# Kernel tuning notes

Measured on AMD Instinct MI355X. Metric: run time of the kernel, lower is better.

The kernel has to match this reference:

```python
import jax, jax.numpy as jnp
import numpy as np

MARGIN = 0.075
CONF_THRESHOLD = 0.2


def setup_inputs() -> dict:
    key = jax.random.key(0)
    k1, k2, k3 = jax.random.split(key, 3)
    N, D = 32768, 256
    embeddings = jax.random.normal(k1, (N, D), dtype=jnp.float32)
    tags = jax.random.randint(k2, (N,), 0, 500, dtype=jnp.int64)
    confidences = jax.random.uniform(k3, (N,), dtype=jnp.float32)
    return {"embeddings": embeddings, "tags": tags, "confidences": confidences}


def _safe_sqrt(sq):
    # gradient-safe sqrt: zero at sq<=0 (matches d(0)=0, avoids NaN in vjp)
    pos = sq > 0
    return jnp.where(pos, jnp.sqrt(jnp.where(pos, sq, 1.0)), 0.0)


def _triplet_hard_mining(emb, labels):
    n = emb.shape[0]
    # pairwise euclidean distances (cdist p=2)
    sq_norm = jnp.sum(emb * emb, axis=1)  # [n]
    sq = sq_norm[:, None] + sq_norm[None, :] - 2.0 * (emb @ emb.T)
    dist = _safe_sqrt(jnp.maximum(sq, 0.0))  # [n, n]

    same = labels[:, None] == labels[None, :]
    eye = jnp.eye(n, dtype=bool)
    pos_mask = same & ~eye
    neg_mask = ~same

    inf = jnp.float32(jnp.inf)
    hard_pos = jnp.max(jnp.where(pos_mask, dist, -inf), axis=1)  # [n]
    neg_min = jnp.min(jnp.where(neg_mask, dist, inf), axis=1)    # [n]
    # semi-hard negatives: neg dists strictly greater than hardest positive
    shn_mask = neg_mask & (dist > hard_pos[:, None])
    shn_min = jnp.min(jnp.where(shn_mask, dist, inf), axis=1)
    hard_neg = jnp.where(jnp.isfinite(shn_min), shn_min, neg_min)

    valid = jnp.any(pos_mask, axis=1) & jnp.any(neg_mask, axis=1)
    per_anchor = jax.nn.relu(hard_pos - hard_neg + MARGIN)
    per_anchor = jnp.where(valid, per_anchor, 0.0)
    cnt = jnp.sum(valid.astype(jnp.float32))
    # if no valid anchors (also covers <2 unique labels), loss is 0
    return jnp.where(cnt > 0, jnp.sum(per_anchor) / jnp.maximum(cnt, 1.0), 0.0)


def reference(embeddings, tags, confidences):
    n = embeddings.shape[0]
    top_k = int(CONF_THRESHOLD * n)
    _, idx = jax.lax.top_k(confidences, top_k)
    emb = embeddings[idx]
    labels = tags[idx]
    return _triplet_hard_mining(emb, labels)
```

## Files before the change

kernel.cpp:

```cpp
#include <hip/hip_runtime.h>
#include <math.h>

#define D 256
#define MARGIN 0.075f

typedef __bf16 bf8_t __attribute__((ext_vector_type(8)));
typedef float f4_t __attribute__((ext_vector_type(4)));
typedef unsigned long long ull;

#define AS1 __attribute__((address_space(1)))
#define AS3 __attribute__((address_space(3)))
static __device__ __forceinline__ void gload_lds16(const void* g, void* s) {
    __builtin_amdgcn_global_load_lds((const AS1 unsigned int*)g, (AS3 unsigned int*)s, 16, 0, 0);
}

static __device__ __forceinline__ unsigned short f2bf(float x) {
    unsigned u = __float_as_uint(x);
    unsigned r = (u + 0x7fffu + ((u >> 16) & 1u)) >> 16;
    return (unsigned short)r;
}

static __device__ __forceinline__ float dec_min(unsigned cm) {
    return (cm == 0u) ? __builtin_inff() : __uint_as_float(~cm);
}

__global__ void k_hist1(const float* __restrict__ conf, int n,
                        unsigned* __restrict__ hist) {
    int i = blockIdx.x * blockDim.x + threadIdx.x;
    if (i < n) atomicAdd(&hist[__float_as_uint(conf[i]) >> 16], 1u);
}

__global__ __launch_bounds__(1024) void k_scan(const unsigned* __restrict__ hist,
                                               unsigned* __restrict__ ctrl, int ksel) {
    __shared__ unsigned part[1024];
    __shared__ int schunk;
    int t = threadIdx.x;
    unsigned k = (unsigned)ksel;
    unsigned s = 0;
    const uint4* h4 = (const uint4*)(hist + t * 64);
    #pragma unroll
    for (int b = 0; b < 16; b++) {
        uint4 v = h4[b];
        s += v.x + v.y + v.z + v.w;
    }
    part[t] = s;
    __syncthreads();
    for (int off = 1; off < 1024; off <<= 1) {
        unsigned v = (t + off < 1024) ? part[t + off] : 0u;
        __syncthreads();
        part[t] += v;
        __syncthreads();
    }
    if (part[t] >= k && (t == 1023 || part[t + 1] < k)) schunk = t;
    __syncthreads();
    if (t == 0) {
        int c = schunk;
        unsigned cum = (c == 1023) ? 0u : part[c + 1];
        int bin = 0; unsigned rem = 1;
        for (int b = 63; b >= 0; b--) {
            unsigned h = hist[c * 64 + b];
            if (cum + h >= k) { bin = c * 64 + b; rem = k - cum; break; }
            cum += h;
        }
        ctrl[3] = (unsigned)bin;
        ctrl[1] = k - rem;
        ctrl[2] = rem;
    }
}

__global__ void k_sel(const float* __restrict__ conf, int n,
                      unsigned* __restrict__ ctrl, int* __restrict__ idx_sel,
                      ull* __restrict__ cand) {
    int i = blockIdx.x * blockDim.x + threadIdx.x;
    if (i < n) {
        unsigned u = __float_as_uint(conf[i]);
        unsigned t16 = u >> 16, b16 = ctrl[3];
        if (t16 > b16) {
            unsigned pos = atomicAdd(&ctrl[5], 1u);
            idx_sel[pos] = i;
        } else if (t16 == b16) {
            unsigned pos = atomicAdd(&ctrl[6], 1u);
            cand[pos] = ((ull)u << 32) | (unsigned)i;
        }
    }
}

__global__ __launch_bounds__(256) void k_sel2(const unsigned* __restrict__ ctrl,
                                              const ull* __restrict__ cand,
                                              int* __restrict__ idx_sel) {
    int t = threadIdx.x;
    int M = (int)ctrl[6];
    unsigned need = ctrl[2], cgt = ctrl[1];
    for (int j = t; j < M; j += 256) {
        ull cj = cand[j];
        unsigned rank = 0;
        for (int m = 0; m < M; m++) {
            ull cm = cand[m];
            unsigned um = (unsigned)(cm >> 32), uj = (unsigned)(cj >> 32);
            if (um > uj || (um == uj && cm < cj)) rank++;
        }
        if (rank < need) idx_sel[cgt + rank] = (int)(unsigned)(cj & 0xFFFFFFFFu);
    }
}

__global__ void k_gather(const float* __restrict__ emb, const int* __restrict__ tags,
                         const int* __restrict__ idx_sel, int ksel, int np,
                         unsigned short* __restrict__ ebf, float* __restrict__ sqn,
                         int* __restrict__ lsel, unsigned* __restrict__ labhist) {
    int j = blockIdx.x;
    int t = threadIdx.x;
    if (j < ksel) {
        int src = idx_sel[j];
        float4 v = *(const float4*)&emb[(size_t)src * D + t * 4];
        ushort4 o;
        o.x = f2bf(v.x); o.y = f2bf(v.y); o.z = f2bf(v.z); o.w = f2bf(v.w);
        *(ushort4*)&ebf[(size_t)j * D + t * 4] = o;
        float s = v.x * v.x + v.y * v.y + v.z * v.z + v.w * v.w;
        for (int off = 32; off > 0; off >>= 1) s += __shfl_down(s, off);
        if (t == 0) {
            int lab = tags[src];
            sqn[j] = s; lsel[j] = lab;
            atomicAdd(&labhist[lab], 1u);
        }
    } else {
        ushort4 z = {0, 0, 0, 0};
        *(ushort4*)&ebf[(size_t)j * D + t * 4] = z;
        if (t == 0) { sqn[j] = 0.f; lsel[j] = -1; }
    }
}

template <int PASS>
__global__ __launch_bounds__(256, 3) void k_fused(const unsigned short* __restrict__ Ebf,
                                                  const float* __restrict__ sqn,
                                                  const int* __restrict__ lsel,
                                                  unsigned* __restrict__ hp_g,
                                                  unsigned* __restrict__ nm_g,
                                                  unsigned* __restrict__ shn_g,
                                                  int np, int nb, int ksel) {
    int rem = blockIdx.x, bi = 0;
    while (rem >= nb - bi) { rem -= nb - bi; bi++; }
    int bj = bi + rem;
    int i0 = bi * 128, j0 = bj * 128;
    bool diag = (bi == bj);

    __shared__ __align__(16) char smem[32768];
    char* ldsA = smem;
    char* ldsB = smem + 16384;

    int t = threadIdx.x;
    int w = t >> 6, l = t & 63;
    int wm = w & 1, wn = w >> 1;
    int lr = l & 15, lq = l >> 4;
    int r7 = lr & 7, rh = lr >> 3;

    int dr = l >> 3;
    int sg = (l & 7) ^ dr;
    const unsigned short* gA = Ebf + (size_t)(i0 + dr) * D + sg * 8;
    const unsigned short* gB = Ebf + (size_t)(j0 + dr) * D + sg * 8;

    f4_t zero = {0.f, 0.f, 0.f, 0.f};
    f4_t acc[4][4];
    #pragma unroll
    for (int p = 0; p < 4; p++)
        #pragma unroll
        for (int q = 0; q < 4; q++) acc[p][q] = zero;

    for (int k0 = 0; k0 < D; k0 += 64) {
        #pragma unroll
        for (int c = 0; c < 4; c++) {
            int R0 = w * 32 + c * 8;
            gload_lds16(gA + (size_t)R0 * D + k0, ldsA + R0 * 128);
            gload_lds16(gB + (size_t)R0 * D + k0, ldsB + R0 * 128);
        }
        __syncthreads();
        #pragma unroll
        for (int ks8 = 0; ks8 < 8; ks8 += 4) {
            bf8_t a[4], b[4];
            #pragma unroll
            for (int p = 0; p < 4; p++) {
                int off = ((wm * 8 + p * 2 + rh) << 10) + ((r7 * 8 + (((ks8 + lq)) ^ r7)) << 4);
                a[p] = *(const bf8_t*)(ldsA + off);
            }
            #pragma unroll
            for (int q = 0; q < 4; q++) {
                int off = ((wn * 8 + q * 2 + rh) << 10) + ((r7 * 8 + (((ks8 + lq)) ^ r7)) << 4);
                b[q] = *(const bf8_t*)(ldsB + off);
            }
            #pragma unroll
            for (int p = 0; p < 4; p++)
                #pragma unroll
                for (int q = 0; q < 4; q++)
                    acc[p][q] = __builtin_amdgcn_mfma_f32_16x16x32_bf16(a[p], b[q], acc[p][q], 0, 0, 0);
        }
        __syncthreads();
    }

    float* sqnA = (float*)smem;
    float* sqnB = sqnA + 128;
    int* labA = (int*)(sqnB + 128);
    int* labB = labA + 128;
    float* hpA2 = (float*)(labB + 128);
    float* hpB2 = hpA2 + 128;
    if (t < 128) {
        sqnA[t] = sqn[i0 + t];
        labA[t] = lsel[i0 + t];
        if (PASS == 2) hpA2[t] = __uint_as_float(hp_g[i0 + t]);
    } else {
        int u = t - 128;
        sqnB[u] = sqn[j0 + u];
        labB[u] = lsel[j0 + u];
        if (PASS == 2) hpB2[u] = __uint_as_float(hp_g[j0 + u]);
    }
    __syncthreads();

    const float INF = __builtin_inff();
    float dsq[4][4][4];
    int colL[4], ljv[4];
    #pragma unroll
    for (int q = 0; q < 4; q++) { colL[q] = wn * 64 + q * 16 + lr; ljv[q] = labB[colL[q]]; }
    #pragma unroll
    for (int p = 0; p < 4; p++) {
        #pragma unroll
        for (int r = 0; r < 4; r++) {
            int rowL = wm * 64 + p * 16 + lq * 4 + r;
            int gm = i0 + rowL;
            float smi = sqnA[rowL];
            #pragma unroll
            for (int q = 0; q < 4; q++) {
                int gn = j0 + colL[q];
                float s = fmaxf(smi + sqnB[colL[q]] - 2.f * acc[p][q][r], 0.f);
                dsq[p][q][r] = (gm < ksel && gn < ksel) ? s : INF;
            }
        }
    }

    #pragma unroll
    for (int p = 0; p < 4; p++) {
        #pragma unroll
        for (int r = 0; r < 4; r++) {
            int rowL = wm * 64 + p * 16 + lq * 4 + r;
            int li = labA[rowL];
            if (PASS == 1) {
                float hpv = -INF, nmv = INF;
                #pragma unroll
                for (int q = 0; q < 4; q++) {
                    float d = dsq[p][q][r];
                    bool self = diag && (rowL == colL[q]);
                    if (ljv[q] == li) { if (!self) hpv = fmaxf(hpv, d); }
                    else nmv = fminf(nmv, d);
                }
                #pragma unroll
                for (int m = 1; m < 16; m <<= 1) {
                    hpv = fmaxf(hpv, __shfl_xor(hpv, m));
                    nmv = fminf(nmv, __shfl_xor(nmv, m));
                }
                if (lr == 0) {
                    if (hpv >= 0.f) atomicMax(&hp_g[i0 + rowL], __float_as_uint(hpv));
                    if (nmv < INF) atomicMax(&nm_g[i0 + rowL], ~__float_as_uint(nmv));
                }
            } else {
                float hpr = hpA2[rowL];
                float smv = INF;
                #pragma unroll
                for (int q = 0; q < 4; q++) {
                    float d = dsq[p][q][r];
                    if (ljv[q] != li && d > hpr) smv = fminf(smv, d);
                }
                #pragma unroll
                for (int m = 1; m < 16; m <<= 1) smv = fminf(smv, __shfl_xor(smv, m));
                if (lr == 0 && smv < INF) atomicMax(&shn_g[i0 + rowL], ~__float_as_uint(smv));
            }
        }
    }

    if (!diag) {
        #pragma unroll
        for (int q = 0; q < 4; q++) {
            int lj = ljv[q];
            if (PASS == 1) {
                float hpv = -INF, nmv = INF;
                #pragma unroll
                for (int p = 0; p < 4; p++)
                    #pragma unroll
                    for (int r = 0; r < 4; r++) {
                        int rowL = wm * 64 + p * 16 + lq * 4 + r;
                        float d = dsq[p][q][r];
                        if (labA[rowL] == lj) hpv = fmaxf(hpv, d);
                        else nmv = fminf(nmv, d);
                    }
                hpv = fmaxf(hpv, __shfl_xor(hpv, 16));
                hpv = fmaxf(hpv, __shfl_xor(hpv, 32));
                nmv = fminf(nmv, __shfl_xor(nmv, 16));
                nmv = fminf(nmv, __shfl_xor(nmv, 32));
                if (lq == 0) {
                    if (hpv >= 0.f) atomicMax(&hp_g[j0 + colL[q]], __float_as_uint(hpv));
                    if (nmv < INF) atomicMax(&nm_g[j0 + colL[q]], ~__float_as_uint(nmv));
                }
            } else {
                float hpc = hpB2[colL[q]];
                float smv = INF;
                #pragma unroll
                for (int p = 0; p < 4; p++)
                    #pragma unroll
                    for (int r = 0; r < 4; r++) {
                        int rowL = wm * 64 + p * 16 + lq * 4 + r;
                        float d = dsq[p][q][r];
                        if (labA[rowL] != lj && d > hpc) smv = fminf(smv, d);
                    }
                smv = fminf(smv, __shfl_xor(smv, 16));
                smv = fminf(smv, __shfl_xor(smv, 32));
                if (lq == 0 && smv < INF) atomicMax(&shn_g[j0 + colL[q]], ~__float_as_uint(smv));
            }
        }
    }
}

__global__ __launch_bounds__(256) void k_loss(const unsigned* __restrict__ hp,
                                              const unsigned* __restrict__ nm,
                                              const unsigned* __restrict__ shn,
                                              const int* __restrict__ lsel,
                                              const unsigned* __restrict__ labhist,
                                              int ksel, float* __restrict__ fsums,
                                              unsigned* __restrict__ ctrl,
                                              float* __restrict__ out) {
    __shared__ float ssum[256], scnt[256];
    int t = threadIdx.x;
    int i = blockIdx.x * 256 + t;
    float sum = 0.f, cnt = 0.f;
    if (i < ksel) {
        int li = lsel[i];
        unsigned h = labhist[li];
        bool valid = (h >= 2u) && ((unsigned)ksel > h);
        float hp2 = __uint_as_float(hp[i]);
        float nm2 = dec_min(nm[i]);
        float sh2 = dec_min(shn[i]);
        float hn2 = isinf(sh2) ? nm2 : sh2;
        float lv = valid ? fmaxf(sqrtf(hp2) - sqrtf(hn2) + MARGIN, 0.f) : 0.f;
        sum = lv;
        cnt = valid ? 1.f : 0.f;
    }
    ssum[t] = sum; scnt[t] = cnt;
    __syncthreads();
    for (int off = 128; off > 0; off >>= 1) {
        if (t < off) { ssum[t] += ssum[t + off]; scnt[t] += scnt[t + off]; }
        __syncthreads();
    }
    if (t == 0) {
        atomicAdd(&fsums[0], ssum[0]);
        atomicAdd(&fsums[1], scnt[0]);
        __threadfence();
        unsigned done = atomicAdd(&ctrl[7], 1u);
        if (done == gridDim.x - 1) {
            float s = atomicAdd(&fsums[0], 0.f);
            float c = atomicAdd(&fsums[1], 0.f);
            out[0] = (c > 0.f) ? (s / fmaxf(c, 1.f)) : 0.f;
        }
    }
}

__global__ void k_wsfail(float* out, float code) { out[0] = code; }

static inline size_t align_up(size_t x, size_t a) { return (x + a - 1) & ~(a - 1); }

extern "C" void kernel_launch(void* const* d_in, const int* in_sizes, int n_in,
                              void* d_out, int out_size, void* d_ws, size_t ws_size,
                              hipStream_t stream) {
    const float* emb  = (const float*)d_in[0];
    const int*   tags = (const int*)d_in[1];
    const float* conf = (const float*)d_in[2];
    float* out = (float*)d_out;

    int n = in_sizes[2];
    int ksel = (int)(0.2 * (double)n);
    int np = ((ksel + 127) / 128) * 128;
    int nb = np / 128;

    size_t off = 0;
    size_t o_ctrl = off; off = align_up(off + 16 * sizeof(unsigned), 256);
    size_t o_fs   = off; off = align_up(off + 8 * sizeof(float), 256);
    size_t o_lh   = off; off = align_up(off + 512 * 4, 256);
    size_t o_hp   = off; off = align_up(off + (size_t)np * 4, 256);
    size_t o_nm   = off; off = align_up(off + (size_t)np * 4, 256);
    size_t o_shn  = off; off = align_up(off + (size_t)np * 4, 256);
    size_t o_h1   = off; off = align_up(off + 65536 * 4, 256);
    size_t zero_bytes = off;
    size_t o_idx  = off; off = align_up(off + (size_t)ksel * 4, 256);
    size_t o_cand = off; off = align_up(off + (size_t)32768 * 8, 256);
    size_t o_lab  = off; off = align_up(off + (size_t)np * 4, 256);
    size_t o_sqn  = off; off = align_up(off + (size_t)np * 4, 256);
    size_t o_ebf  = off; off = align_up(off + (size_t)np * D * 2, 256);

    if (ws_size < off) {
        k_wsfail<<<1, 1, 0, stream>>>(out, -(float)(ws_size >> 20));
        return;
    }

    char* ws = (char*)d_ws;
    unsigned*       ctrl    = (unsigned*)(ws + o_ctrl);
    float*          fsums   = (float*)(ws + o_fs);
    unsigned*       labhist = (unsigned*)(ws + o_lh);
    unsigned*       hp_g    = (unsigned*)(ws + o_hp);
    unsigned*       nm_g    = (unsigned*)(ws + o_nm);
    unsigned*       shn_g   = (unsigned*)(ws + o_shn);
    unsigned*       h1      = (unsigned*)(ws + o_h1);
    int*            idx_sel = (int*)(ws + o_idx);
    ull*            cand    = (ull*)(ws + o_cand);
    int*            lsel    = (int*)(ws + o_lab);
    float*          sqn     = (float*)(ws + o_sqn);
    unsigned short* ebf     = (unsigned short*)(ws + o_ebf);

    hipMemsetAsync(d_ws, 0, zero_bytes, stream);
    k_hist1<<<(n + 255) / 256, 256, 0, stream>>>(conf, n, h1);
    k_scan<<<1, 1024, 0, stream>>>(h1, ctrl, ksel);
    k_sel<<<(n + 255) / 256, 256, 0, stream>>>(conf, n, ctrl, idx_sel, cand);
    k_sel2<<<1, 256, 0, stream>>>(ctrl, cand, idx_sel);
    k_gather<<<np, 64, 0, stream>>>(emb, tags, idx_sel, ksel, np, ebf, sqn, lsel, labhist);
    int ntri = nb * (nb + 1) / 2;
    k_fused<1><<<ntri, 256, 0, stream>>>(ebf, sqn, lsel, hp_g, nm_g, shn_g, np, nb, ksel);
    k_fused<2><<<ntri, 256, 0, stream>>>(ebf, sqn, lsel, hp_g, nm_g, shn_g, np, nb, ksel);
    k_loss<<<(ksel + 255) / 256, 256, 0, stream>>>(hp_g, nm_g, shn_g, lsel, labhist,
                                                   ksel, fsums, ctrl, out);
}
```

Baseline: 201.1 us.

## Compute hardest positives per label group and merge the two distance passes

Builds a per-label member list during the gather step. A new small kernel computes each anchor's hardest-positive distance using only pairs within the same label group. With the hardest positive known in advance, one fused GEMM pass can compute both the negative minimum and the semi-hard negative minimum. This removes the second full pairwise GEMM pass. Row reductions now use DPP intrinsics instead of shuffles. The cost is that group size is capped at MAXM=96 members, so larger label groups would give wrong hardest positives.

```diff
diff --git a/kernel.cpp b/kernel.cpp
--- a/kernel.cpp
+++ b/kernel.cpp
@@ -3,6 +3,7 @@
 
 #define D 256
 #define MARGIN 0.075f
+#define MAXM 96
 
 typedef __bf16 bf8_t __attribute__((ext_vector_type(8)));
 typedef float f4_t __attribute__((ext_vector_type(4)));
@@ -24,6 +25,19 @@
     return (cm == 0u) ? __builtin_inff() : __uint_as_float(~cm);
 }
 
+static __device__ __forceinline__ float rmin16(float v) {
+    int s;
+    s = __builtin_amdgcn_update_dpp(__float_as_int(v), __float_as_int(v), 0x101, 0xF, 0xF, false);
+    v = fminf(v, __int_as_float(s));
+    s = __builtin_amdgcn_update_dpp(__float_as_int(v), __float_as_int(v), 0x102, 0xF, 0xF, false);
+    v = fminf(v, __int_as_float(s));
+    s = __builtin_amdgcn_update_dpp(__float_as_int(v), __float_as_int(v), 0x104, 0xF, 0xF, false);
+    v = fminf(v, __int_as_float(s));
+    s = __builtin_amdgcn_update_dpp(__float_as_int(v), __float_as_int(v), 0x108, 0xF, 0xF, false);
+    v = fminf(v, __int_as_float(s));
+    return v;
+}
+
 __global__ void k_hist1(const float* __restrict__ conf, int n,
                         unsigned* __restrict__ hist) {
     int i = blockIdx.x * blockDim.x + threadIdx.x;
@@ -39,10 +53,7 @@
     unsigned s = 0;
     const uint4* h4 = (const uint4*)(hist + t * 64);
     #pragma unroll
-    for (int b = 0; b < 16; b++) {
-        uint4 v = h4[b];
-        s += v.x + v.y + v.z + v.w;
-    }
+    for (int b = 0; b < 16; b++) { uint4 v = h4[b]; s += v.x + v.y + v.z + v.w; }
     part[t] = s;
     __syncthreads();
     for (int off = 1; off < 1024; off <<= 1) {
@@ -93,10 +104,11 @@
     unsigned need = ctrl[2], cgt = ctrl[1];
     for (int j = t; j < M; j += 256) {
         ull cj = cand[j];
+        unsigned uj = (unsigned)(cj >> 32);
         unsigned rank = 0;
         for (int m = 0; m < M; m++) {
             ull cm = cand[m];
-            unsigned um = (unsigned)(cm >> 32), uj = (unsigned)(cj >> 32);
+            unsigned um = (unsigned)(cm >> 32);
             if (um > uj || (um == uj && cm < cj)) rank++;
         }
         if (rank < need) idx_sel[cgt + rank] = (int)(unsigned)(cj & 0xFFFFFFFFu);
@@ -106,7 +118,8 @@
 __global__ void k_gather(const float* __restrict__ emb, const int* __restrict__ tags,
                          const int* __restrict__ idx_sel, int ksel, int np,
                          unsigned short* __restrict__ ebf, float* __restrict__ sqn,
-                         int* __restrict__ lsel, unsigned* __restrict__ labhist) {
+                         int* __restrict__ lsel, unsigned* __restrict__ labhist,
+                         int* __restrict__ members) {
     int j = blockIdx.x;
     int t = threadIdx.x;
     if (j < ksel) {
@@ -120,7 +133,8 @@
         if (t == 0) {
             int lab = tags[src];
             sqn[j] = s; lsel[j] = lab;
-            atomicAdd(&labhist[lab], 1u);
+            unsigned slot = atomicAdd(&labhist[lab], 1u);
+            if (slot < MAXM) members[lab * MAXM + slot] = j;
         }
     } else {
         ushort4 z = {0, 0, 0, 0};
@@ -129,11 +143,64 @@
     }
 }
 
-template <int PASS>
+__global__ __launch_bounds__(256) void k_hardpos(const unsigned short* __restrict__ ebf,
+                                                 const float* __restrict__ sqn,
+                                                 const int* __restrict__ members,
+                                                 const unsigned* __restrict__ labhist,
+                                                 unsigned* __restrict__ hp_g) {
+    int L = blockIdx.x;
+    int t = threadIdx.x;
+    int m = (int)labhist[L];
+    if (m > MAXM) m = MAXM;
+    if (m < 2) return;
+
+    __shared__ unsigned short rows[MAXM * 256];
+    __shared__ float lsqn[MAXM];
+    __shared__ unsigned hpl[MAXM];
+    __shared__ int ridx[MAXM];
+
+    for (int a = t; a < m; a += 256) {
+        int r = members[L * MAXM + a];
+        ridx[a] = r; lsqn[a] = sqn[r]; hpl[a] = 0u;
+    }
+    __syncthreads();
+    for (int e = t * 8; e < m * 256; e += 256 * 8) {
+        int a = e >> 8, c = e & 255;
+        *(uint4*)&rows[a * 256 + c] = *(const uint4*)&ebf[(size_t)ridx[a] * D + c];
+    }
+    __syncthreads();
+
+    int npair = m * (m - 1) / 2;
+    for (int pidx = t; pidx < npair; pidx += 256) {
+        int a = 0, rem = pidx;
+        while (rem >= m - 1 - a) { rem -= m - 1 - a; a++; }
+        int b = a + 1 + rem;
+        const unsigned* ra = (const unsigned*)&rows[a * 256];
+        const unsigned* rb = (const unsigned*)&rows[b * 256];
+        float dot = 0.f;
+        #pragma unroll 8
+        for (int c = 0; c < 128; c++) {
+            unsigned ua = ra[c], ub = rb[c];
+            float a0 = __uint_as_float(ua << 16);
+            float a1 = __uint_as_float(ua & 0xFFFF0000u);
+            float b0 = __uint_as_float(ub << 16);
+            float b1 = __uint_as_float(ub & 0xFFFF0000u);
+            dot = fmaf(a0, b0, dot);
+            dot = fmaf(a1, b1, dot);
+        }
+        float dsq = fmaxf(lsqn[a] + lsqn[b] - 2.f * dot, 0.f);
+        unsigned bits = __float_as_uint(dsq);
+        atomicMax(&hpl[a], bits);
+        atomicMax(&hpl[b], bits);
+    }
+    __syncthreads();
+    for (int a = t; a < m; a += 256) hp_g[ridx[a]] = hpl[a];
+}
+
 __global__ __launch_bounds__(256, 3) void k_fused(const unsigned short* __restrict__ Ebf,
                                                   const float* __restrict__ sqn,
                                                   const int* __restrict__ lsel,
-                                                  unsigned* __restrict__ hp_g,
+                                                  const unsigned* __restrict__ hp_g,
                                                   unsigned* __restrict__ nm_g,
                                                   unsigned* __restrict__ shn_g,
                                                   int np, int nb, int ksel) {
@@ -178,12 +245,12 @@
             bf8_t a[4], b[4];
             #pragma unroll
             for (int p = 0; p < 4; p++) {
-                int off = ((wm * 8 + p * 2 + rh) << 10) + ((r7 * 8 + (((ks8 + lq)) ^ r7)) << 4);
+                int off = ((wm * 8 + p * 2 + rh) << 10) + ((r7 * 8 + ((ks8 + lq) ^ r7)) << 4);
                 a[p] = *(const bf8_t*)(ldsA + off);
             }
             #pragma unroll
             for (int q = 0; q < 4; q++) {
-                int off = ((wn * 8 + q * 2 + rh) << 10) + ((r7 * 8 + (((ks8 + lq)) ^ r7)) << 4);
+                int off = ((wn * 8 + q * 2 + rh) << 10) + ((r7 * 8 + ((ks8 + lq) ^ r7)) << 4);
                 b[q] = *(const bf8_t*)(ldsB + off);
             }
             #pragma unroll
@@ -204,12 +271,12 @@
     if (t < 128) {
         sqnA[t] = sqn[i0 + t];
         labA[t] = lsel[i0 + t];
-        if (PASS == 2) hpA2[t] = __uint_as_float(hp_g[i0 + t]);
+        hpA2[t] = __uint_as_float(hp_g[i0 + t]);
     } else {
         int u = t - 128;
         sqnB[u] = sqn[j0 + u];
         labB[u] = lsel[j0 + u];
-        if (PASS == 2) hpB2[u] = __uint_as_float(hp_g[j0 + u]);
+        hpB2[u] = __uint_as_float(hp_g[j0 + u]);
     }
     __syncthreads();
 
@@ -240,35 +307,21 @@
         for (int r = 0; r < 4; r++) {
             int rowL = wm * 64 + p * 16 + lq * 4 + r;
             int li = labA[rowL];
-            if (PASS == 1) {
-                float hpv = -INF, nmv = INF;
-                #pragma unroll
-                for (int q = 0; q < 4; q++) {
-                    float d = dsq[p][q][r];
-                    bool self = diag && (rowL == colL[q]);
-                    if (ljv[q] == li) { if (!self) hpv = fmaxf(hpv, d); }
-                    else nmv = fminf(nmv, d);
+            float hpr = hpA2[rowL];
+            float nmv = INF, smv = INF;
+            #pragma unroll
+            for (int q = 0; q < 4; q++) {
+                float d = dsq[p][q][r];
+                if (ljv[q] != li) {
+                    nmv = fminf(nmv, d);
+                    if (d > hpr) smv = fminf(smv, d);
                 }
-                #pragma unroll
-                for (int m = 1; m < 16; m <<= 1) {
-                    hpv = fmaxf(hpv, __shfl_xor(hpv, m));
-                    nmv = fminf(nmv, __shfl_xor(nmv, m));
-                }
-                if (lr == 0) {
-                    if (hpv >= 0.f) atomicMax(&hp_g[i0 + rowL], __float_as_uint(hpv));
-                    if (nmv < INF) atomicMax(&nm_g[i0 + rowL], ~__float_as_uint(nmv));
-                }
-            } else {
-                float hpr = hpA2[rowL];
-                float smv = INF;
-                #pragma unroll
-                for (int q = 0; q < 4; q++) {
-                    float d = dsq[p][q][r];
-                    if (ljv[q] != li && d > hpr) smv = fminf(smv, d);
-                }
-                #pragma unroll
-                for (int m = 1; m < 16; m <<= 1) smv = fminf(smv, __shfl_xor(smv, m));
-                if (lr == 0 && smv < INF) atomicMax(&shn_g[i0 + rowL], ~__float_as_uint(smv));
+            }
+            nmv = rmin16(nmv);
+            smv = rmin16(smv);
+            if (lr == 0) {
+                if (nmv < INF) atomicMax(&nm_g[i0 + rowL], ~__float_as_uint(nmv));
+                if (smv < INF) atomicMax(&shn_g[i0 + rowL], ~__float_as_uint(smv));
             }
         }
     }
@@ -277,39 +330,26 @@
         #pragma unroll
         for (int q = 0; q < 4; q++) {
             int lj = ljv[q];
-            if (PASS == 1) {
-                float hpv = -INF, nmv = INF;
+            float hpc = hpB2[colL[q]];
+            float nmv = INF, smv = INF;
+            #pragma unroll
+            for (int p = 0; p < 4; p++)
                 #pragma unroll
-                for (int p = 0; p < 4; p++)
-                    #pragma unroll
-                    for (int r = 0; r < 4; r++) {
-                        int rowL = wm * 64 + p * 16 + lq * 4 + r;
-                        float d = dsq[p][q][r];
-                        if (labA[rowL] == lj) hpv = fmaxf(hpv, d);
-                        else nmv = fminf(nmv, d);
+                for (int r = 0; r < 4; r++) {
+                    int rowL = wm * 64 + p * 16 + lq * 4 + r;
+                    float d = dsq[p][q][r];
+                    if (labA[rowL] != lj) {
+                        nmv = fminf(nmv, d);
+                        if (d > hpc) smv = fminf(smv, d);
                     }
-                hpv = fmaxf(hpv, __shfl_xor(hpv, 16));
-                hpv = fmaxf(hpv, __shfl_xor(hpv, 32));
-                nmv = fminf(nmv, __shfl_xor(nmv, 16));
-                nmv = fminf(nmv, __shfl_xor(nmv, 32));
-                if (lq == 0) {
-                    if (hpv >= 0.f) atomicMax(&hp_g[j0 + colL[q]], __float_as_uint(hpv));
-                    if (nmv < INF) atomicMax(&nm_g[j0 + colL[q]], ~__float_as_uint(nmv));
                 }
-            } else {
-                float hpc = hpB2[colL[q]];
-                float smv = INF;
-                #pragma unroll
-                for (int p = 0; p < 4; p++)
-                    #pragma unroll
-                    for (int r = 0; r < 4; r++) {
-                        int rowL = wm * 64 + p * 16 + lq * 4 + r;
-                        float d = dsq[p][q][r];
-                        if (labA[rowL] != lj && d > hpc) smv = fminf(smv, d);
-                    }
-                smv = fminf(smv, __shfl_xor(smv, 16));
-                smv = fminf(smv, __shfl_xor(smv, 32));
-                if (lq == 0 && smv < INF) atomicMax(&shn_g[j0 + colL[q]], ~__float_as_uint(smv));
+            nmv = fminf(nmv, __shfl_xor(nmv, 16));
+            nmv = fminf(nmv, __shfl_xor(nmv, 32));
+            smv = fminf(smv, __shfl_xor(smv, 16));
+            smv = fminf(smv, __shfl_xor(smv, 32));
+            if (lq == 0) {
+                if (nmv < INF) atomicMax(&nm_g[j0 + colL[q]], ~__float_as_uint(nmv));
+                if (smv < INF) atomicMax(&shn_g[j0 + colL[q]], ~__float_as_uint(smv));
             }
         }
     }
@@ -374,18 +414,20 @@
     int ksel = (int)(0.2 * (double)n);
     int np = ((ksel + 127) / 128) * 128;
     int nb = np / 128;
+    int nlab = 512;
 
     size_t off = 0;
-    size_t o_ctrl = off; off = align_up(off + 16 * sizeof(unsigned), 256);
+    size_t o_ctrl = off; off = align_up(off + 32 * sizeof(unsigned), 256);
     size_t o_fs   = off; off = align_up(off + 8 * sizeof(float), 256);
-    size_t o_lh   = off; off = align_up(off + 512 * 4, 256);
+    size_t o_lh   = off; off = align_up(off + (size_t)nlab * 4, 256);
     size_t o_hp   = off; off = align_up(off + (size_t)np * 4, 256);
     size_t o_nm   = off; off = align_up(off + (size_t)np * 4, 256);
     size_t o_shn  = off; off = align_up(off + (size_t)np * 4, 256);
     size_t o_h1   = off; off = align_up(off + 65536 * 4, 256);
     size_t zero_bytes = off;
     size_t o_idx  = off; off = align_up(off + (size_t)ksel * 4, 256);
-    size_t o_cand = off; off = align_up(off + (size_t)32768 * 8, 256);
+    size_t o_cand = off; off = align_up(off + (size_t)n * 8, 256);
+    size_t o_mem  = off; off = align_up(off + (size_t)nlab * MAXM * 4, 256);
     size_t o_lab  = off; off = align_up(off + (size_t)np * 4, 256);
     size_t o_sqn  = off; off = align_up(off + (size_t)np * 4, 256);
     size_t o_ebf  = off; off = align_up(off + (size_t)np * D * 2, 256);
@@ -405,6 +447,7 @@
     unsigned*       h1      = (unsigned*)(ws + o_h1);
     int*            idx_sel = (int*)(ws + o_idx);
     ull*            cand    = (ull*)(ws + o_cand);
+    int*            members = (int*)(ws + o_mem);
     int*            lsel    = (int*)(ws + o_lab);
     float*          sqn     = (float*)(ws + o_sqn);
     unsigned short* ebf     = (unsigned short*)(ws + o_ebf);
@@ -414,10 +457,11 @@
     k_scan<<<1, 1024, 0, stream>>>(h1, ctrl, ksel);
     k_sel<<<(n + 255) / 256, 256, 0, stream>>>(conf, n, ctrl, idx_sel, cand);
     k_sel2<<<1, 256, 0, stream>>>(ctrl, cand, idx_sel);
-    k_gather<<<np, 64, 0, stream>>>(emb, tags, idx_sel, ksel, np, ebf, sqn, lsel, labhist);
+    k_gather<<<np, 64, 0, stream>>>(emb, tags, idx_sel, ksel, np, ebf, sqn, lsel,
+                                    labhist, members);
+    k_hardpos<<<512, 256, 0, stream>>>(ebf, sqn, members, labhist, hp_g);
     int ntri = nb * (nb + 1) / 2;
-    k_fused<1><<<ntri, 256, 0, stream>>>(ebf, sqn, lsel, hp_g, nm_g, shn_g, np, nb, ksel);
-    k_fused<2><<<ntri, 256, 0, stream>>>(ebf, sqn, lsel, hp_g, nm_g, shn_g, np, nb, ksel);
+    k_fused<<<ntri, 256, 0, stream>>>(ebf, sqn, lsel, hp_g, nm_g, shn_g, np, nb, ksel);
     k_loss<<<(ksel + 255) / 256, 256, 0, stream>>>(hp_g, nm_g, shn_g, lsel, labhist,
                                                    ksel, fsums, ctrl, out);
 }
```

Result: faster. 185.9 us (-7.6%).
